# Optimization experiments

Hardware: AMD Instinct MI355X
Metric: run time of the kernel (lower is better)

Reference implementation:

```python
import jax, jax.numpy as jnp
import numpy as np

N = 262144
DIM = 256
NUM_HEADS = 4
HEAD_DIM = DIM // NUM_HEADS
B = 4096
SCALE = HEAD_DIM ** (-0.5)
EPS = 1e-8


def setup_inputs() -> dict:
    key = jax.random.key(0)
    ks = jax.random.split(key, 7)
    x = jax.random.normal(ks[0], (N, DIM), dtype=jnp.float32)
    batch = jnp.sort(jax.random.randint(ks[1], (N,), 0, B)).astype(jnp.int64)
    query = jax.random.normal(ks[2], (NUM_HEADS, HEAD_DIM), dtype=jnp.float32)
    # nn.Linear default init scale ~ 1/sqrt(dim); keep exp() well-behaved
    key_w = jax.random.normal(ks[3], (DIM, DIM), dtype=jnp.float32) / np.sqrt(DIM)
    key_b = jax.random.normal(ks[4], (DIM,), dtype=jnp.float32) * 0.01
    value_w = jax.random.normal(ks[5], (DIM, DIM), dtype=jnp.float32) / np.sqrt(DIM)
    value_b = jax.random.normal(ks[6], (DIM,), dtype=jnp.float32) * 0.01
    return {"x": x, "batch": batch, "query": query, "key_w": key_w,
            "key_b": key_b, "value_w": value_w, "value_b": value_b}


def reference(x, batch, query, key_w, key_b, value_w, value_b):
    # k, v: [N, H, Hd]  (torch Linear: x @ W.T + b)
    k = (x @ key_w.T + key_b).reshape(N, NUM_HEADS, HEAD_DIM)
    v = (x @ value_w.T + value_b).reshape(N, NUM_HEADS, HEAD_DIM)
    # attn: [N, H] -- dot of learned per-head query with each node's key
    attn = jnp.einsum('hd,nhd->nh', query, k) * SCALE
    attn_exp = jnp.exp(attn)  # faithful: no max-subtraction in original
    # segment softmax denominator gathered back to nodes: [N, H]
    attn_sum = jax.ops.segment_sum(attn_exp, batch, num_segments=B)[batch]
    attn_norm = attn_exp / (attn_sum + EPS)
    # weighted values scatter-added per segment: [B, H, Hd]
    weighted = attn_norm[:, :, None] * v
    pooled = jax.ops.segment_sum(weighted, batch, num_segments=B)
    return pooled.reshape(B, DIM)
```

## Files before the change

### kernel.cpp

```cpp
#include <hip/hip_runtime.h>


constexpr int DIM = 256;
constexpr int NH  = 4;
constexpr int HD  = 64;
constexpr float SCL  = 0.125f;
constexpr float EPSV = 1e-8f;

constexpr int WS_QW   = 0;
constexpr int WS_QB   = 1024;
constexpr int WS_OFFS = 1088;
constexpr int WS_VWT  = 8192;
constexpr int WS_SRAW = 73728;

__global__ void prep_qw(const float* __restrict__ query,
                        const float* __restrict__ key_w,
                        const float* __restrict__ key_b,
                        float* __restrict__ ws){
  int t = blockIdx.x * 256 + threadIdx.x;
  int h = t >> 8, j = t & 255;
  float acc = 0.f;
  #pragma unroll 8
  for (int d = 0; d < HD; ++d)
    acc += query[h*HD+d] * key_w[(size_t)(h*HD+d)*DIM + j];
  ws[WS_QW + t] = acc;
  if (j == 0){
    float bb = 0.f;
    for (int d = 0; d < HD; ++d)
      bb += query[h*HD+d] * key_b[h*HD+d];
    ws[WS_QB + h] = bb;
  }
}

__global__ void prep_vwt(const float* __restrict__ value_w, float* __restrict__ ws){
  int jj = blockIdx.x;
  int t  = threadIdx.x;
  float4 v = *(const float4*)(value_w + (size_t)t*DIM + 4*jj);
  ((float4*)(ws + WS_VWT))[jj*256 + t] = v;
}

__global__ void seg_offsets(const int* __restrict__ batch32,
                            int* __restrict__ offs, int N, int B){
  int i = blockIdx.x * 256 + threadIdx.x;
  if (i >= N) return;
  const bool is64 = (batch32[N-1] == 0);
  int v  = is64 ? batch32[2*i] : batch32[i];
  int vp = (i == 0) ? -1 : (is64 ? batch32[2*(i-1)] : batch32[i-1]);
  for (int b = vp + 1; b <= v; ++b) offs[b] = i;
  if (i == N-1)
    for (int b = v + 1; b <= B; ++b) offs[b] = N;
}

__global__ __launch_bounds__(256, 4)
void attn_pool3(const float* __restrict__ x,
                const int* __restrict__ offs,
                const float* __restrict__ ws,
                float* __restrict__ sraw,
                float* __restrict__ esum){
  __shared__ __align__(16) float S_all[4][NH*DIM];
  __shared__ float sums_all[4][NH];

  const int b   = blockIdx.x;
  const int tid = threadIdx.x;
  const int s = offs[b], e = offs[b+1];

  const int wave = tid >> 6, lane = tid & 63;

  float qwr[NH][4];
  #pragma unroll
  for (int h = 0; h < NH; ++h){
    float4 q = *(const float4*)(ws + WS_QW + h*DIM + 4*lane);
    qwr[h][0]=q.x; qwr[h][1]=q.y; qwr[h][2]=q.z; qwr[h][3]=q.w;
  }
  float qb[NH];
  #pragma unroll
  for (int h = 0; h < NH; ++h) qb[h] = ws[WS_QB + h];

  float Sacc[NH][4];
  #pragma unroll
  for (int h = 0; h < NH; ++h)
    #pragma unroll
    for (int c = 0; c < 4; ++c) Sacc[h][c] = 0.f;
  float se[NH] = {0.f, 0.f, 0.f, 0.f};

  const float4* xr4 = (const float4*)x;

  int n0 = s + (wave << 2);
  float4 A[4]; bool g[4];
  #pragma unroll
  for (int i = 0; i < 4; ++i){
    g[i] = (n0 + i) < e;
    const int safe = g[i] ? (n0 + i) : 0;
    A[i] = xr4[(size_t)safe * 64 + lane];
  }

  while (n0 < e){
    const int nn = n0 + 16;
    float4 An[4]; bool gn[4];
    #pragma unroll
    for (int i = 0; i < 4; ++i){
      gn[i] = (nn + i) < e;
      const int safe = gn[i] ? (nn + i) : 0;
      An[i] = xr4[(size_t)safe * 64 + lane];
    }

    float p[4][NH];
    #pragma unroll
    for (int i = 0; i < 4; ++i)
      #pragma unroll
      for (int h = 0; h < NH; ++h)
        p[i][h] = qwr[h][0]*A[i].x + qwr[h][1]*A[i].y
                + qwr[h][2]*A[i].z + qwr[h][3]*A[i].w;

    #pragma unroll
    for (int m = 1; m < 64; m <<= 1){
      #pragma unroll
      for (int i = 0; i < 4; ++i)
        #pragma unroll
        for (int h = 0; h < NH; ++h)
          p[i][h] += __shfl_xor(p[i][h], m, 64);
    }

    #pragma unroll
    for (int i = 0; i < 4; ++i){
      #pragma unroll
      for (int h = 0; h < NH; ++h){
        const float ev = g[i] ? __expf((p[i][h] + qb[h]) * SCL) : 0.f;
        se[h] += ev;
        Sacc[h][0] += ev * A[i].x;
        Sacc[h][1] += ev * A[i].y;
        Sacc[h][2] += ev * A[i].z;
        Sacc[h][3] += ev * A[i].w;
      }
    }

    n0 = nn;
    #pragma unroll
    for (int i = 0; i < 4; ++i){ A[i] = An[i]; g[i] = gn[i]; }
  }

  #pragma unroll
  for (int h = 0; h < NH; ++h)
    *(float4*)&S_all[wave][h*DIM + 4*lane] =
        make_float4(Sacc[h][0], Sacc[h][1], Sacc[h][2], Sacc[h][3]);
  if (lane == 0){
    #pragma unroll
    for (int h = 0; h < NH; ++h) sums_all[wave][h] = se[h];
  }
  __syncthreads();

  #pragma unroll
  for (int k = 0; k < 4; ++k){
    const int idx = tid + k*256;
    const float sv = S_all[0][idx] + S_all[1][idx] + S_all[2][idx] + S_all[3][idx];
    sraw[(size_t)b*1024 + idx] = sv;
  }
  if (tid < NH){
    esum[b*4 + tid] = sums_all[0][tid] + sums_all[1][tid]
                    + sums_all[2][tid] + sums_all[3][tid];
  }
}

__global__ __launch_bounds__(256, 4)
void val_proj(const float* __restrict__ ws,
              const float* __restrict__ sraw,
              const float* __restrict__ esum,
              const float* __restrict__ value_b,
              float* __restrict__ out){
  constexpr int TB  = 8;
  constexpr int TBP = 9;
  __shared__ __align__(16) float Sl[NH*DIM*TBP];
  const int b0  = blockIdx.x * TB;
  const int tid = threadIdx.x;

  for (int idx = tid; idx < NH*DIM*TB; idx += 256){
    const int i = idx >> 10, rem = idx & 1023;
    Sl[rem*TBP + i] = sraw[(size_t)(b0 + i)*1024 + rem];
  }
  __syncthreads();

  const int t = tid, h = t >> 6;
  const float4* vwt4 = (const float4*)(ws + WS_VWT);
  float acc[TB];
  #pragma unroll
  for (int i = 0; i < TB; ++i) acc[i] = 0.f;

  #pragma unroll 4
  for (int jj = 0; jj < 64; ++jj){
    const float4 w4 = vwt4[jj*256 + t];
    #pragma unroll
    for (int r = 0; r < 4; ++r){
      const float* sp = &Sl[(h*256 + 4*jj + r)*TBP];
      const float wr = (&w4.x)[r];
      acc[0] += wr*sp[0]; acc[1] += wr*sp[1]; acc[2] += wr*sp[2]; acc[3] += wr*sp[3];
      acc[4] += wr*sp[4]; acc[5] += wr*sp[5]; acc[6] += wr*sp[6]; acc[7] += wr*sp[7];
    }
  }
  const float vb = value_b[t];
  #pragma unroll
  for (int i = 0; i < TB; ++i){
    const float es  = esum[(b0 + i)*4 + h];
    const float inv = 1.f / (es + EPSV);
    out[(size_t)(b0 + i)*256 + t] = acc[i]*inv + es*inv*vb;
  }
}

template<int MODE>
__global__ __launch_bounds__(512, 4)
void attn_pool_fused(const float* __restrict__ x,
                     const int* __restrict__ offs,
                     const float* __restrict__ ws,
                     const float* __restrict__ value_w,
                     const float* __restrict__ value_b,
                     float* __restrict__ out){
  constexpr int LDSF = (MODE == 1) ? (8192 + 32 + 1024 + 2048 + 8)
                                   : (8192 + 32 + 1024 + 512 + 8);
  __shared__ __align__(16) float lds[LDSF];
  float* S_all    = lds;
  float* sums_all = lds + 8192;

  const int b   = blockIdx.x;
  const int tid = threadIdx.x;
  const int seg_start = offs[b];
  const int seg_end   = offs[b+1];

  const int wave = tid >> 6, lane = tid & 63;
  const int half = lane >> 5, sl = lane & 31;
  const int sigma = wave * 2 + half;

  float qwr[NH][8];
  #pragma unroll
  for (int h = 0; h < NH; ++h){
    float4 a = *(const float4*)(ws + WS_QW + h*DIM + 4*sl);
    float4 c = *(const float4*)(ws + WS_QW + h*DIM + 128 + 4*sl);
    qwr[h][0]=a.x; qwr[h][1]=a.y; qwr[h][2]=a.z; qwr[h][3]=a.w;
    qwr[h][4]=c.x; qwr[h][5]=c.y; qwr[h][6]=c.z; qwr[h][7]=c.w;
  }
  float qb[NH];
  #pragma unroll
  for (int h = 0; h < NH; ++h) qb[h] = ws[WS_QB + h];

  float Sacc[NH][8];
  #pragma unroll
  for (int h = 0; h < NH; ++h)
    #pragma unroll
    for (int c = 0; c < 8; ++c) Sacc[h][c] = 0.f;
  float se[NH] = {0.f, 0.f, 0.f, 0.f};

  const float4* xr4 = (const float4*)x;
  const float4 Z = make_float4(0.f,0.f,0.f,0.f);

  int n0 = seg_start + sigma*2;
  bool v0 = n0 < seg_end;
  bool v1 = n0 + 1 < seg_end;
  float4 a0=Z, b0=Z, a1=Z, b1=Z;
  if (v0){ a0 = xr4[(size_t)n0*64 + sl];     b0 = xr4[(size_t)n0*64 + 32 + sl]; }
  if (v1){ a1 = xr4[(size_t)(n0+1)*64 + sl]; b1 = xr4[(size_t)(n0+1)*64 + 32 + sl]; }

  while (v0){
    const int nn = n0 + 32;
    const bool w0 = nn < seg_end;
    const bool w1 = nn + 1 < seg_end;
    float4 c0=Z, d0=Z, c1=Z, d1=Z;
    if (w0){ c0 = xr4[(size_t)nn*64 + sl];     d0 = xr4[(size_t)nn*64 + 32 + sl]; }
    if (w1){ c1 = xr4[(size_t)(nn+1)*64 + sl]; d1 = xr4[(size_t)(nn+1)*64 + 32 + sl]; }

    float xv0[8] = {a0.x,a0.y,a0.z,a0.w,b0.x,b0.y,b0.z,b0.w};
    float xv1[8] = {a1.x,a1.y,a1.z,a1.w,b1.x,b1.y,b1.z,b1.w};

    float p0[NH], p1[NH];
    #pragma unroll
    for (int h = 0; h < NH; ++h){
      float s0 = 0.f, s1 = 0.f;
      #pragma unroll
      for (int c = 0; c < 8; ++c){ s0 += qwr[h][c]*xv0[c]; s1 += qwr[h][c]*xv1[c]; }
      p0[h] = s0; p1[h] = s1;
    }
    #pragma unroll
    for (int m = 1; m < 32; m <<= 1){
      #pragma unroll
      for (int h = 0; h < NH; ++h){
        p0[h] += __shfl_xor(p0[h], m, 64);
        p1[h] += __shfl_xor(p1[h], m, 64);
      }
    }
    const float g1 = v1 ? 1.f : 0.f;
    #pragma unroll
    for (int h = 0; h < NH; ++h){
      float e0 = __expf((p0[h] + qb[h]) * SCL);
      float e1 = __expf((p1[h] + qb[h]) * SCL) * g1;
      se[h] += e0 + e1;
      #pragma unroll
      for (int c = 0; c < 8; ++c)
        Sacc[h][c] += e0*xv0[c] + e1*xv1[c];
    }
    n0 = nn; v0 = w0; v1 = w1;
    a0 = c0; b0 = d0; a1 = c1; b1 = d1;
  }

  #pragma unroll
  for (int h = 0; h < NH; ++h){
    se[h] += __shfl_xor(se[h], 32, 64);
    #pragma unroll
    for (int c = 0; c < 8; ++c) Sacc[h][c] += __shfl_xor(Sacc[h][c], 32, 64);
  }
  if (half == 0){
    #pragma unroll
    for (int h = 0; h < NH; ++h){
      float4 lo = make_float4(Sacc[h][0], Sacc[h][1], Sacc[h][2], Sacc[h][3]);
      float4 hi = make_float4(Sacc[h][4], Sacc[h][5], Sacc[h][6], Sacc[h][7]);
      *(float4*)&S_all[wave*1024 + h*DIM + 4*sl]       = lo;
      *(float4*)&S_all[wave*1024 + h*DIM + 128 + 4*sl] = hi;
    }
    if (sl == 0){
      #pragma unroll
      for (int h = 0; h < NH; ++h) sums_all[wave*4 + h] = se[h];
    }
  }
  __syncthreads();

  float* Sfin  = lds + 8224;
  float* invs  = (MODE == 1) ? lds + 11296 : lds + 9760;
  float* wsums = invs + 4;
  #pragma unroll
  for (int k = 0; k < 2; ++k){
    const int idx = tid + k*512;
    float sv = 0.f;
    #pragma unroll
    for (int w = 0; w < 8; ++w) sv += S_all[w*1024 + idx];
    Sfin[idx] = sv;
  }
  if (tid < NH){
    float tot = 0.f;
    #pragma unroll
    for (int w = 0; w < 8; ++w) tot += sums_all[w*4 + tid];
    float inv = 1.f / (tot + EPSV);
    invs[tid] = inv; wsums[tid] = tot * inv;
  }
  __syncthreads();

  if constexpr (MODE == 1){
    float* ep = lds + 9248;
    const float4* vwt4 = (const float4*)(ws + WS_VWT);
    const int hh = lane >> 4;
    float4 acc = make_float4(0.f, 0.f, 0.f, 0.f);
    for (int jj = wave*8; jj < wave*8 + 8; ++jj){
      float4 q0 = vwt4[jj*256 + 4*lane + 0];
      float4 q1 = vwt4[jj*256 + 4*lane + 1];
      float4 q2 = vwt4[jj*256 + 4*lane + 2];
      float4 q3 = vwt4[jj*256 + 4*lane + 3];
      float4 sf = *(const float4*)&Sfin[hh*256 + 4*jj];
      acc.x += q0.x*sf.x + q0.y*sf.y + q0.z*sf.z + q0.w*sf.w;
      acc.y += q1.x*sf.x + q1.y*sf.y + q1.z*sf.z + q1.w*sf.w;
      acc.z += q2.x*sf.x + q2.y*sf.y + q2.z*sf.z + q2.w*sf.w;
      acc.w += q3.x*sf.x + q3.y*sf.y + q3.z*sf.z + q3.w*sf.w;
    }
    *(float4*)&ep[wave*256 + 4*lane] = acc;
    __syncthreads();
    if (tid < 256){
      const int t = tid, h2 = t >> 6;
      float sv = 0.f;
      #pragma unroll
      for (int w = 0; w < 8; ++w) sv += ep[w*256 + t];
      out[(size_t)b*256 + t] = sv * invs[h2] + wsums[h2] * value_b[t];
    }
  } else {
    float* ep2 = lds + 9248;
    const int t = tid & 255, part = tid >> 8;
    const int h2 = t >> 6;
    const float4* vrow = (const float4*)(value_w + (size_t)t * DIM) + part*32;
    const float4* sp   = (const float4*)&Sfin[h2*256] + part*32;
    float acc = 0.f;
    #pragma unroll
    for (int q = 0; q < 32; ++q){
      float4 r = vrow[q];
      float4 sv = sp[q];
      acc += r.x*sv.x + r.y*sv.y + r.z*sv.z + r.w*sv.w;
    }
    ep2[part*256 + t] = acc;
    __syncthreads();
    if (part == 0)
      out[(size_t)b * DIM + t] = (ep2[t] + ep2[256 + t]) * invs[h2] + wsums[h2] * value_b[t];
  }
}

extern "C" void kernel_launch(void* const* d_in, const int* in_sizes, int n_in,
                              void* d_out, int out_size, void* d_ws, size_t ws_size,
                              hipStream_t stream){
  const float* x       = (const float*)d_in[0];
  const int*   batch   = (const int*)d_in[1];
  const float* query   = (const float*)d_in[2];
  const float* key_w   = (const float*)d_in[3];
  const float* key_b   = (const float*)d_in[4];
  const float* value_w = (const float*)d_in[5];
  const float* value_b = (const float*)d_in[6];
  float* ws  = (float*)d_ws;
  float* out = (float*)d_out;

  const int N = in_sizes[1];
  const int B = out_size / DIM;

  int*   offs = (int*)(ws + WS_OFFS);
  float* sraw = ws + WS_SRAW;
  float* esum = ws + WS_SRAW + (size_t)B*1024;

  const size_t need_split = ((size_t)WS_SRAW + (size_t)B*1024 + (size_t)B*4) * sizeof(float);
  const size_t need_vwt   = ((size_t)WS_VWT + 65536) * sizeof(float);

  prep_qw<<<4, 256, 0, stream>>>(query, key_w, key_b, ws);
  seg_offsets<<<(N + 255) / 256, 256, 0, stream>>>(batch, offs, N, B);

  if (ws_size >= need_split){
    prep_vwt<<<64, 256, 0, stream>>>(value_w, ws);
    attn_pool3<<<B, 256, 0, stream>>>(x, offs, ws, sraw, esum);
    val_proj<<<B / 8, 256, 0, stream>>>(ws, sraw, esum, value_b, out);
  } else if (ws_size >= need_vwt){
    prep_vwt<<<64, 256, 0, stream>>>(value_w, ws);
    attn_pool_fused<1><<<B, 512, 0, stream>>>(x, offs, ws, value_w, value_b, out);
  } else {
    attn_pool_fused<2><<<B, 512, 0, stream>>>(x, offs, ws, value_w, value_b, out);
  }
}
```

Baseline: 418.0 us.

## Stream fixed row chunks per wave with atomic segment flush instead of per-segment blocks

```diff
diff --git a/kernel.cpp b/kernel.cpp
--- a/kernel.cpp
+++ b/kernel.cpp
@@ -13,30 +13,35 @@
 constexpr int WS_VWT  = 8192;
 constexpr int WS_SRAW = 73728;
 
-__global__ void prep_qw(const float* __restrict__ query,
-                        const float* __restrict__ key_w,
-                        const float* __restrict__ key_b,
-                        float* __restrict__ ws){
-  int t = blockIdx.x * 256 + threadIdx.x;
-  int h = t >> 8, j = t & 255;
-  float acc = 0.f;
-  #pragma unroll 8
-  for (int d = 0; d < HD; ++d)
-    acc += query[h*HD+d] * key_w[(size_t)(h*HD+d)*DIM + j];
-  ws[WS_QW + t] = acc;
-  if (j == 0){
-    float bb = 0.f;
+__global__ void prep_all(const float* __restrict__ query,
+                         const float* __restrict__ key_w,
+                         const float* __restrict__ key_b,
+                         const float* __restrict__ value_w,
+                         float* __restrict__ ws, int zero_f4){
+  const int bid = blockIdx.x, tid = threadIdx.x;
+  if (bid < 64){
+    float4 v = *(const float4*)(value_w + (size_t)tid*DIM + 4*bid);
+    ((float4*)(ws + WS_VWT))[bid*256 + tid] = v;
+  } else if (bid < 68){
+    int t = (bid - 64)*256 + tid;
+    int h = t >> 8, j = t & 255;
+    float acc = 0.f;
+    #pragma unroll 8
     for (int d = 0; d < HD; ++d)
-      bb += query[h*HD+d] * key_b[h*HD+d];
-    ws[WS_QB + h] = bb;
-  }
-}
-
-__global__ void prep_vwt(const float* __restrict__ value_w, float* __restrict__ ws){
-  int jj = blockIdx.x;
-  int t  = threadIdx.x;
-  float4 v = *(const float4*)(value_w + (size_t)t*DIM + 4*jj);
-  ((float4*)(ws + WS_VWT))[jj*256 + t] = v;
+      acc += query[h*HD+d] * key_w[(size_t)(h*HD+d)*DIM + j];
+    ws[WS_QW + t] = acc;
+    if (j == 0){
+      float bb = 0.f;
+      for (int d = 0; d < HD; ++d)
+        bb += query[h*HD+d] * key_b[h*HD+d];
+      ws[WS_QB + h] = bb;
+    }
+  } else {
+    float4* z = (float4*)(ws + WS_SRAW);
+    const int stride = (gridDim.x - 68) * 256;
+    for (int i = (bid - 68)*256 + tid; i < zero_f4; i += stride)
+      z[i] = make_float4(0.f, 0.f, 0.f, 0.f);
+  }
 }
 
 __global__ void seg_offsets(const int* __restrict__ batch32,
@@ -52,19 +57,21 @@
 }
 
 __global__ __launch_bounds__(256, 4)
-void attn_pool3(const float* __restrict__ x,
-                const int* __restrict__ offs,
-                const float* __restrict__ ws,
-                float* __restrict__ sraw,
-                float* __restrict__ esum){
-  __shared__ __align__(16) float S_all[4][NH*DIM];
-  __shared__ float sums_all[4][NH];
-
-  const int b   = blockIdx.x;
-  const int tid = threadIdx.x;
-  const int s = offs[b], e = offs[b+1];
-
+void attn_stream(const float* __restrict__ x,
+                 const int* __restrict__ batch32,
+                 const float* __restrict__ ws,
+                 float* __restrict__ sraw,
+                 float* __restrict__ esum,
+                 int N, int rpw){
+  const int tid  = threadIdx.x;
   const int wave = tid >> 6, lane = tid & 63;
+  const int gid  = blockIdx.x * 4 + wave;
+  const int start = gid * rpw;
+  if (start >= N) return;
+  const int end = (start + rpw < N) ? (start + rpw) : N;
+
+  const bool is64 = (batch32[N-1] == 0);
+  const int bstr  = is64 ? 2 : 1;
 
   float qwr[NH][4];
   #pragma unroll
@@ -81,28 +88,47 @@
   for (int h = 0; h < NH; ++h)
     #pragma unroll
     for (int c = 0; c < 4; ++c) Sacc[h][c] = 0.f;
-  float se[NH] = {0.f, 0.f, 0.f, 0.f};
+  float se0 = 0.f, se1 = 0.f, se2 = 0.f, se3 = 0.f;
+
+  int cur = batch32[(size_t)start * bstr];
+
+  auto flushfn = [&](int seg){
+    #pragma unroll
+    for (int h = 0; h < NH; ++h){
+      float* bp = sraw + (size_t)seg*1024 + h*256 + 4*lane;
+      atomicAdd(bp + 0, Sacc[h][0]);
+      atomicAdd(bp + 1, Sacc[h][1]);
+      atomicAdd(bp + 2, Sacc[h][2]);
+      atomicAdd(bp + 3, Sacc[h][3]);
+      Sacc[h][0]=Sacc[h][1]=Sacc[h][2]=Sacc[h][3]=0.f;
+    }
+    float v = (lane == 0) ? se0 : (lane == 1) ? se1 : (lane == 2) ? se2 : se3;
+    if (lane < NH) atomicAdd(esum + seg*4 + lane, v);
+    se0 = se1 = se2 = se3 = 0.f;
+  };
 
   const float4* xr4 = (const float4*)x;
 
-  int n0 = s + (wave << 2);
-  float4 A[4]; bool g[4];
+  int n0 = start;
+  float4 A[4];
   #pragma unroll
   for (int i = 0; i < 4; ++i){
-    g[i] = (n0 + i) < e;
-    const int safe = g[i] ? (n0 + i) : 0;
-    A[i] = xr4[(size_t)safe * 64 + lane];
-  }
-
-  while (n0 < e){
-    const int nn = n0 + 16;
-    float4 An[4]; bool gn[4];
+    int n = n0 + i; n = (n < N-1) ? n : (N-1);
+    A[i] = xr4[(size_t)n * 64 + lane];
+  }
+
+  while (n0 < end){
+    const int nn = n0 + 4;
+    float4 An[4];
     #pragma unroll
     for (int i = 0; i < 4; ++i){
-      gn[i] = (nn + i) < e;
-      const int safe = gn[i] ? (nn + i) : 0;
-      An[i] = xr4[(size_t)safe * 64 + lane];
-    }
+      int n = nn + i; n = (n < N-1) ? n : (N-1);
+      An[i] = xr4[(size_t)n * 64 + lane];
+    }
+    int sg[4];
+    #pragma unroll
+    for (int i = 0; i < 4; ++i)
+      sg[i] = batch32[(size_t)(n0 + i) * bstr];
 
     float p[4][NH];
     #pragma unroll
@@ -123,42 +149,23 @@
 
     #pragma unroll
     for (int i = 0; i < 4; ++i){
-      #pragma unroll
-      for (int h = 0; h < NH; ++h){
-        const float ev = g[i] ? __expf((p[i][h] + qb[h]) * SCL) : 0.f;
-        se[h] += ev;
-        Sacc[h][0] += ev * A[i].x;
-        Sacc[h][1] += ev * A[i].y;
-        Sacc[h][2] += ev * A[i].z;
-        Sacc[h][3] += ev * A[i].w;
-      }
+      if (sg[i] != cur){ flushfn(cur); cur = sg[i]; }
+      const float e0 = __expf((p[i][0] + qb[0]) * SCL);
+      const float e1 = __expf((p[i][1] + qb[1]) * SCL);
+      const float e2 = __expf((p[i][2] + qb[2]) * SCL);
+      const float e3 = __expf((p[i][3] + qb[3]) * SCL);
+      se0 += e0; se1 += e1; se2 += e2; se3 += e3;
+      Sacc[0][0]+=e0*A[i].x; Sacc[0][1]+=e0*A[i].y; Sacc[0][2]+=e0*A[i].z; Sacc[0][3]+=e0*A[i].w;
+      Sacc[1][0]+=e1*A[i].x; Sacc[1][1]+=e1*A[i].y; Sacc[1][2]+=e1*A[i].z; Sacc[1][3]+=e1*A[i].w;
+      Sacc[2][0]+=e2*A[i].x; Sacc[2][1]+=e2*A[i].y; Sacc[2][2]+=e2*A[i].z; Sacc[2][3]+=e2*A[i].w;
+      Sacc[3][0]+=e3*A[i].x; Sacc[3][1]+=e3*A[i].y; Sacc[3][2]+=e3*A[i].z; Sacc[3][3]+=e3*A[i].w;
     }
 
     n0 = nn;
     #pragma unroll
-    for (int i = 0; i < 4; ++i){ A[i] = An[i]; g[i] = gn[i]; }
-  }
-
-  #pragma unroll
-  for (int h = 0; h < NH; ++h)
-    *(float4*)&S_all[wave][h*DIM + 4*lane] =
-        make_float4(Sacc[h][0], Sacc[h][1], Sacc[h][2], Sacc[h][3]);
-  if (lane == 0){
-    #pragma unroll
-    for (int h = 0; h < NH; ++h) sums_all[wave][h] = se[h];
-  }
-  __syncthreads();
-
-  #pragma unroll
-  for (int k = 0; k < 4; ++k){
-    const int idx = tid + k*256;
-    const float sv = S_all[0][idx] + S_all[1][idx] + S_all[2][idx] + S_all[3][idx];
-    sraw[(size_t)b*1024 + idx] = sv;
-  }
-  if (tid < NH){
-    esum[b*4 + tid] = sums_all[0][tid] + sums_all[1][tid]
-                    + sums_all[2][tid] + sums_all[3][tid];
-  }
+    for (int i = 0; i < 4; ++i) A[i] = An[i];
+  }
+  flushfn(cur);
 }
 
 __global__ __launch_bounds__(256, 4)
@@ -400,24 +407,26 @@
   const int N = in_sizes[1];
   const int B = out_size / DIM;
 
-  int*   offs = (int*)(ws + WS_OFFS);
   float* sraw = ws + WS_SRAW;
   float* esum = ws + WS_SRAW + (size_t)B*1024;
 
-  const size_t need_split = ((size_t)WS_SRAW + (size_t)B*1024 + (size_t)B*4) * sizeof(float);
+  const size_t need_split = ((size_t)WS_SRAW + (size_t)B*1028) * sizeof(float);
   const size_t need_vwt   = ((size_t)WS_VWT + 65536) * sizeof(float);
 
-  prep_qw<<<4, 256, 0, stream>>>(query, key_w, key_b, ws);
-  seg_offsets<<<(N + 255) / 256, 256, 0, stream>>>(batch, offs, N, B);
-
   if (ws_size >= need_split){
-    prep_vwt<<<64, 256, 0, stream>>>(value_w, ws);
-    attn_pool3<<<B, 256, 0, stream>>>(x, offs, ws, sraw, esum);
+    const int zero_f4 = B * 257;
+    prep_all<<<68 + 1024, 256, 0, stream>>>(query, key_w, key_b, value_w, ws, zero_f4);
+    const int rpw = 32;
+    const int nblocks = (N + rpw*4 - 1) / (rpw*4);
+    attn_stream<<<nblocks, 256, 0, stream>>>(x, batch, ws, sraw, esum, N, rpw);
     val_proj<<<B / 8, 256, 0, stream>>>(ws, sraw, esum, value_b, out);
-  } else if (ws_size >= need_vwt){
-    prep_vwt<<<64, 256, 0, stream>>>(value_w, ws);
-    attn_pool_fused<1><<<B, 512, 0, stream>>>(x, offs, ws, value_w, value_b, out);
   } else {
-    attn_pool_fused<2><<<B, 512, 0, stream>>>(x, offs, ws, value_w, value_b, out);
-  }
-}
+    int* offs = (int*)(ws + WS_OFFS);
+    prep_all<<<68, 256, 0, stream>>>(query, key_w, key_b, value_w, ws, 0);
+    seg_offsets<<<(N + 255) / 256, 256, 0, stream>>>(batch, offs, N, B);
+    if (ws_size >= need_vwt)
+      attn_pool_fused<1><<<B, 512, 0, stream>>>(x, offs, ws, value_w, value_b, out);
+    else
+      attn_pool_fused<2><<<B, 512, 0, stream>>>(x, offs, ws, value_w, value_b, out);
+  }
+}
```

Result: slower. 514.1 us (+23.0%).

## Deepen x prefetch to 8-row double buffers and merge prep kernels

Applied to the files above, without the earlier changes.

```diff
diff --git a/kernel.cpp b/kernel.cpp
--- a/kernel.cpp
+++ b/kernel.cpp
@@ -13,30 +13,30 @@
 constexpr int WS_VWT  = 8192;
 constexpr int WS_SRAW = 73728;
 
-__global__ void prep_qw(const float* __restrict__ query,
-                        const float* __restrict__ key_w,
-                        const float* __restrict__ key_b,
-                        float* __restrict__ ws){
-  int t = blockIdx.x * 256 + threadIdx.x;
-  int h = t >> 8, j = t & 255;
-  float acc = 0.f;
-  #pragma unroll 8
-  for (int d = 0; d < HD; ++d)
-    acc += query[h*HD+d] * key_w[(size_t)(h*HD+d)*DIM + j];
-  ws[WS_QW + t] = acc;
-  if (j == 0){
-    float bb = 0.f;
+__global__ void prep_all(const float* __restrict__ query,
+                         const float* __restrict__ key_w,
+                         const float* __restrict__ key_b,
+                         const float* __restrict__ value_w,
+                         float* __restrict__ ws){
+  const int bid = blockIdx.x, tid = threadIdx.x;
+  if (bid < 64){
+    float4 v = *(const float4*)(value_w + (size_t)tid*DIM + 4*bid);
+    ((float4*)(ws + WS_VWT))[bid*256 + tid] = v;
+  } else {
+    int t = (bid - 64)*256 + tid;
+    int h = t >> 8, j = t & 255;
+    float acc = 0.f;
+    #pragma unroll 8
     for (int d = 0; d < HD; ++d)
-      bb += query[h*HD+d] * key_b[h*HD+d];
-    ws[WS_QB + h] = bb;
-  }
-}
-
-__global__ void prep_vwt(const float* __restrict__ value_w, float* __restrict__ ws){
-  int jj = blockIdx.x;
-  int t  = threadIdx.x;
-  float4 v = *(const float4*)(value_w + (size_t)t*DIM + 4*jj);
-  ((float4*)(ws + WS_VWT))[jj*256 + t] = v;
+      acc += query[h*HD+d] * key_w[(size_t)(h*HD+d)*DIM + j];
+    ws[WS_QW + t] = acc;
+    if (j == 0){
+      float bb = 0.f;
+      for (int d = 0; d < HD; ++d)
+        bb += query[h*HD+d] * key_b[h*HD+d];
+      ws[WS_QB + h] = bb;
+    }
+  }
 }
 
 __global__ void seg_offsets(const int* __restrict__ batch32,
@@ -51,8 +51,8 @@
     for (int b = v + 1; b <= B; ++b) offs[b] = N;
 }
 
-__global__ __launch_bounds__(256, 4)
-void attn_pool3(const float* __restrict__ x,
+__global__ __launch_bounds__(256, 3)
+void attn_chunk(const float* __restrict__ x,
                 const int* __restrict__ offs,
                 const float* __restrict__ ws,
                 float* __restrict__ sraw,
@@ -63,7 +63,6 @@
   const int b   = blockIdx.x;
   const int tid = threadIdx.x;
   const int s = offs[b], e = offs[b+1];
-
   const int wave = tid >> 6, lane = tid & 63;
 
   float qwr[NH][4];
@@ -84,59 +83,64 @@
   float se[NH] = {0.f, 0.f, 0.f, 0.f};
 
   const float4* xr4 = (const float4*)x;
-
-  int n0 = s + (wave << 2);
-  float4 A[4]; bool g[4];
-  #pragma unroll
-  for (int i = 0; i < 4; ++i){
-    g[i] = (n0 + i) < e;
-    const int safe = g[i] ? (n0 + i) : 0;
-    A[i] = xr4[(size_t)safe * 64 + lane];
-  }
-
-  while (n0 < e){
-    const int nn = n0 + 16;
-    float4 An[4]; bool gn[4];
-    #pragma unroll
-    for (int i = 0; i < 4; ++i){
-      gn[i] = (nn + i) < e;
-      const int safe = gn[i] ? (nn + i) : 0;
-      An[i] = xr4[(size_t)safe * 64 + lane];
-    }
-
-    float p[4][NH];
-    #pragma unroll
-    for (int i = 0; i < 4; ++i)
-      #pragma unroll
-      for (int h = 0; h < NH; ++h)
-        p[i][h] = qwr[h][0]*A[i].x + qwr[h][1]*A[i].y
-                + qwr[h][2]*A[i].z + qwr[h][3]*A[i].w;
-
-    #pragma unroll
-    for (int m = 1; m < 64; m <<= 1){
-      #pragma unroll
-      for (int i = 0; i < 4; ++i)
+  const float4 Z = make_float4(0.f, 0.f, 0.f, 0.f);
+
+  auto compute8 = [&](const float4* Bv, int base){
+    #pragma unroll
+    for (int sb = 0; sb < 2; ++sb){
+      float p[4][NH];
+      #pragma unroll
+      for (int i = 0; i < 4; ++i){
+        const float4 A = Bv[4*sb + i];
         #pragma unroll
         for (int h = 0; h < NH; ++h)
-          p[i][h] += __shfl_xor(p[i][h], m, 64);
-    }
-
-    #pragma unroll
-    for (int i = 0; i < 4; ++i){
-      #pragma unroll
-      for (int h = 0; h < NH; ++h){
-        const float ev = g[i] ? __expf((p[i][h] + qb[h]) * SCL) : 0.f;
-        se[h] += ev;
-        Sacc[h][0] += ev * A[i].x;
-        Sacc[h][1] += ev * A[i].y;
-        Sacc[h][2] += ev * A[i].z;
-        Sacc[h][3] += ev * A[i].w;
+          p[i][h] = qwr[h][0]*A.x + qwr[h][1]*A.y + qwr[h][2]*A.z + qwr[h][3]*A.w;
       }
-    }
-
+      #pragma unroll
+      for (int m = 1; m < 64; m <<= 1){
+        #pragma unroll
+        for (int i = 0; i < 4; ++i)
+          #pragma unroll
+          for (int h = 0; h < NH; ++h)
+            p[i][h] += __shfl_xor(p[i][h], m, 64);
+      }
+      #pragma unroll
+      for (int i = 0; i < 4; ++i){
+        const float4 A = Bv[4*sb + i];
+        const bool gv = (base + 4*sb + i) < e;
+        #pragma unroll
+        for (int h = 0; h < NH; ++h){
+          const float ev = gv ? __expf((p[i][h] + qb[h]) * SCL) : 0.f;
+          se[h] += ev;
+          Sacc[h][0] += ev * A.x;
+          Sacc[h][1] += ev * A.y;
+          Sacc[h][2] += ev * A.z;
+          Sacc[h][3] += ev * A.w;
+        }
+      }
+    }
+  };
+
+  int n0 = s + wave*8;
+  float4 B0[8], B1[8];
+  #pragma unroll
+  for (int i = 0; i < 8; ++i)
+    B0[i] = (n0 + i < e) ? xr4[(size_t)(n0+i)*64 + lane] : Z;
+
+  while (n0 < e){
+    const int nn = n0 + 32;
+    #pragma unroll
+    for (int i = 0; i < 8; ++i)
+      B1[i] = (nn + i < e) ? xr4[(size_t)(nn+i)*64 + lane] : Z;
+    compute8(B0, n0);
     n0 = nn;
-    #pragma unroll
-    for (int i = 0; i < 4; ++i){ A[i] = An[i]; g[i] = gn[i]; }
+    if (n0 >= e) break;
+    const int nm = n0 + 32;
+    #pragma unroll
+    for (int i = 0; i < 8; ++i)
+      B0[i] = (nm + i < e) ? xr4[(size_t)(nm+i)*64 + lane] : Z;
+    compute8(B1, n0);
+    n0 = nm;
   }
 
   #pragma unroll
@@ -205,7 +209,6 @@
   }
 }
 
-template<int MODE>
 __global__ __launch_bounds__(512, 4)
 void attn_pool_fused(const float* __restrict__ x,
                      const int* __restrict__ offs,
@@ -213,9 +216,7 @@
                      const float* __restrict__ value_w,
                      const float* __restrict__ value_b,
                      float* __restrict__ out){
-  constexpr int LDSF = (MODE == 1) ? (8192 + 32 + 1024 + 2048 + 8)
-                                   : (8192 + 32 + 1024 + 512 + 8);
-  __shared__ __align__(16) float lds[LDSF];
+  __shared__ __align__(16) float lds[8192 + 32 + 1024 + 512 + 8];
   float* S_all    = lds;
   float* sums_all = lds + 8192;
 
@@ -320,7 +321,7 @@
   __syncthreads();
 
   float* Sfin  = lds + 8224;
-  float* invs  = (MODE == 1) ? lds + 11296 : lds + 9760;
+  float* invs  = lds + 9760;
   float* wsums = invs + 4;
   #pragma unroll
   for (int k = 0; k < 2; ++k){
@@ -339,49 +340,22 @@
   }
   __syncthreads();
 
-  if constexpr (MODE == 1){
-    float* ep = lds + 9248;
-    const float4* vwt4 = (const float4*)(ws + WS_VWT);
-    const int hh = lane >> 4;
-    float4 acc = make_float4(0.f, 0.f, 0.f, 0.f);
-    for (int jj = wave*8; jj < wave*8 + 8; ++jj){
-      float4 q0 = vwt4[jj*256 + 4*lane + 0];
-      float4 q1 = vwt4[jj*256 + 4*lane + 1];
-      float4 q2 = vwt4[jj*256 + 4*lane + 2];
-      float4 q3 = vwt4[jj*256 + 4*lane + 3];
-      float4 sf = *(const float4*)&Sfin[hh*256 + 4*jj];
-      acc.x += q0.x*sf.x + q0.y*sf.y + q0.z*sf.z + q0.w*sf.w;
-      acc.y += q1.x*sf.x + q1.y*sf.y + q1.z*sf.z + q1.w*sf.w;
-      acc.z += q2.x*sf.x + q2.y*sf.y + q2.z*sf.z + q2.w*sf.w;
-      acc.w += q3.x*sf.x + q3.y*sf.y + q3.z*sf.z + q3.w*sf.w;
-    }
-    *(float4*)&ep[wave*256 + 4*lane] = acc;
-    __syncthreads();
-    if (tid < 256){
-      const int t = tid, h2 = t >> 6;
-      float sv = 0.f;
-      #pragma unroll
-      for (int w = 0; w < 8; ++w) sv += ep[w*256 + t];
-      out[(size_t)b*256 + t] = sv * invs[h2] + wsums[h2] * value_b[t];
-    }
-  } else {
-    float* ep2 = lds + 9248;
-    const int t = tid & 255, part = tid >> 8;
-    const int h2 = t >> 6;
-    const float4* vrow = (const float4*)(value_w + (size_t)t * DIM) + part*32;
-    const float4* sp   = (const float4*)&Sfin[h2*256] + part*32;
-    float acc = 0.f;
-    #pragma unroll
-    for (int q = 0; q < 32; ++q){
-      float4 r = vrow[q];
-      float4 sv = sp[q];
-      acc += r.x*sv.x + r.y*sv.y + r.z*sv.z + r.w*sv.w;
-    }
-    ep2[part*256 + t] = acc;
-    __syncthreads();
-    if (part == 0)
-      out[(size_t)b * DIM + t] = (ep2[t] + ep2[256 + t]) * invs[h2] + wsums[h2] * value_b[t];
-  }
+  float* ep2 = lds + 9248;
+  const int t = tid & 255, part = tid >> 8;
+  const int h2 = t >> 6;
+  const float4* vrow = (const float4*)(value_w + (size_t)t * DIM) + part*32;
+  const float4* sp   = (const float4*)&Sfin[h2*256] + part*32;
+  float acc = 0.f;
+  #pragma unroll
+  for (int q = 0; q < 32; ++q){
+    float4 r = vrow[q];
+    float4 sv = sp[q];
+    acc += r.x*sv.x + r.y*sv.y + r.z*sv.z + r.w*sv.w;
+  }
+  ep2[part*256 + t] = acc;
+  __syncthreads();
+  if (part == 0)
+    out[(size_t)b * DIM + t] = (ep2[t] + ep2[256 + t]) * invs[h2] + wsums[h2] * value_b[t];
 }
 
 extern "C" void kernel_launch(void* const* d_in, const int* in_sizes, int n_in,
@@ -404,20 +378,15 @@
   float* sraw = ws + WS_SRAW;
   float* esum = ws + WS_SRAW + (size_t)B*1024;
 
-  const size_t need_split = ((size_t)WS_SRAW + (size_t)B*1024 + (size_t)B*4) * sizeof(float);
-  const size_t need_vwt   = ((size_t)WS_VWT + 65536) * sizeof(float);
-
-  prep_qw<<<4, 256, 0, stream>>>(query, key_w, key_b, ws);
+  const size_t need_split = ((size_t)WS_SRAW + (size_t)B*1028) * sizeof(float);
+
+  prep_all<<<68, 256, 0, stream>>>(query, key_w, key_b, value_w, ws);
   seg_offsets<<<(N + 255) / 256, 256, 0, stream>>>(batch, offs, N, B);
 
   if (ws_size >= need_split){
-    prep_vwt<<<64, 256, 0, stream>>>(value_w, ws);
-    attn_pool3<<<B, 256, 0, stream>>>(x, offs, ws, sraw, esum);
+    attn_chunk<<<B, 256, 0, stream>>>(x, offs, ws, sraw, esum);
     val_proj<<<B / 8, 256, 0, stream>>>(ws, sraw, esum, value_b, out);
-  } else if (ws_size >= need_vwt){
-    prep_vwt<<<64, 256, 0, stream>>>(value_w, ws);
-    attn_pool_fused<1><<<B, 512, 0, stream>>>(x, offs, ws, value_w, value_b, out);
   } else {
-    attn_pool_fused<2><<<B, 512, 0, stream>>>(x, offs, ws, value_w, value_b, out);
-  }
-}
+    attn_pool_fused<<<B, 512, 0, stream>>>(x, offs, ws, value_w, value_b, out);
+  }
+}
```

New measurement: 446.4 us. +6.8%, slower.
